# Kernel tuning notes

Hardware: AMD Instinct MI355X
Metric: run time of the kernel (lower is better)

Reference implementation:

```python
import jax, jax.numpy as jnp
import numpy as np

IN_CH = 1024
HID_CH = 1024
NUM_HEADS = 16
HEAD_DIM = HID_CH // NUM_HEADS
SCALE = (HID_CH / NUM_HEADS) ** (-0.25)


def _xavier(key, shape):
    fan_out, fan_in = shape
    limit = np.sqrt(6.0 / (fan_in + fan_out)).astype(np.float32)
    return jax.random.uniform(key, shape, jnp.float32, -limit, limit)


def setup_inputs() -> dict:
    key = jax.random.key(0)
    ks = jax.random.split(key, 5)
    B, T, L = 4, 2048, 512
    inpt = jax.random.normal(ks[0], (B, IN_CH, T), jnp.float32)
    aux = jax.random.normal(ks[1], (L, IN_CH), jnp.float32)
    q_w = _xavier(ks[2], (HID_CH, IN_CH))
    q_b = jnp.zeros((HID_CH,), jnp.float32)
    kv_w = _xavier(ks[3], (2 * HID_CH, IN_CH))
    kv_b = jnp.zeros((2 * HID_CH,), jnp.float32)
    out_w = _xavier(ks[4], (IN_CH, HID_CH))
    out_b = jnp.zeros((IN_CH,), jnp.float32)
    return {"inpt": inpt, "aux": aux, "q_w": q_w, "q_b": q_b,
            "kv_w": kv_w, "kv_b": kv_b, "out_w": out_w, "out_b": out_b}


def reference(inpt, aux, q_w, q_b, kv_w, kv_b, out_w, out_b):
    # inpt: (B, C, T), aux: (L, C)
    B, C, T = inpt.shape
    x = jnp.swapaxes(inpt, -2, -1)                     # (B, T, C)
    q = (x @ q_w.T + q_b) * SCALE                      # (B, T, H*D)
    kv = aux @ kv_w.T + kv_b                           # (L, 2*H*D)
    k, v = jnp.split(kv, 2, axis=-1)
    k = k * SCALE
    q = q.reshape(B, T, NUM_HEADS, HEAD_DIM)           # (B, T, h, d)
    L = aux.shape[0]
    k = k.reshape(L, NUM_HEADS, HEAD_DIM)              # (L, h, d)
    v = v.reshape(L, NUM_HEADS, HEAD_DIM)
    e = jnp.einsum('bihd,jhd->bijh', q, k)             # (B, T, L, h)
    attn = jax.nn.softmax(e, axis=2)                   # softmax over key axis j
    out = jnp.einsum('bijh,jhd->bihd', attn, v)        # (B, T, h, d)
    out = out.reshape(B, T, HID_CH) @ out_w.T + out_b  # (B, T, C)
    return inpt + jnp.swapaxes(out, -2, -1)            # (B, C, T)
```

## Files before the change

kernel.cpp:

```cpp
#include <hip/hip_runtime.h>
#include <cstdint>
#include <cstddef>

typedef __bf16 bf16;
typedef __bf16 bf16x4 __attribute__((ext_vector_type(4)));
typedef __bf16 bf16x8 __attribute__((ext_vector_type(8)));
typedef float f32x4 __attribute__((ext_vector_type(4)));

static constexpr float SCALE_F = 0.35355339059327373f;

#define AS1 __attribute__((address_space(1)))
#define AS3 __attribute__((address_space(3)))

__device__ __forceinline__ void load_lds16(const void* g, void* l) {
  __builtin_amdgcn_global_load_lds((AS1 void*)g, (AS3 void*)l, 16, 0, 0);
}

__global__ void prep(const float* __restrict__ q_w, bf16* __restrict__ qwb,
                     const float* __restrict__ kv_w, bf16* __restrict__ kvwb,
                     const float* __restrict__ out_w, bf16* __restrict__ owb,
                     const float* __restrict__ aux, bf16* __restrict__ auxb,
                     const float* __restrict__ inpt, bf16* __restrict__ X) {
  const int bid = blockIdx.x;
  const int tid = threadIdx.x;
  if (bid < 4608) {
    int i = bid * 256 + tid;
    const float* src;
    bf16* dst;
    int off;
    if (i < 262144) { src = q_w; dst = qwb; off = i; }
    else if (i < 786432) { src = kv_w; dst = kvwb; off = i - 262144; }
    else if (i < 1048576) { src = out_w; dst = owb; off = i - 786432; }
    else { src = aux; dst = auxb; off = i - 1048576; }
    float4 v = reinterpret_cast<const float4*>(src)[off];
    bf16x4 o;
    o[0] = (bf16)v.x; o[1] = (bf16)v.y; o[2] = (bf16)v.z; o[3] = (bf16)v.w;
    reinterpret_cast<bf16x4*>(dst)[off] = o;
  } else {
    __shared__ float tile[32][33];
    int tb = bid - 4608;
    int b = tb >> 11;
    int rem = tb & 2047;
    int c0 = (rem >> 6) * 32;
    int t0 = (rem & 63) * 32;
    int tx = tid & 31, ty = tid >> 5;
    const float* src = inpt + ((size_t)b * 1024 + c0) * 2048 + t0;
#pragma unroll
    for (int i = 0; i < 4; ++i) tile[ty + i * 8][tx] = src[(size_t)(ty + i * 8) * 2048 + tx];
    __syncthreads();
    bf16* dst = X + ((size_t)b * 2048 + t0) * 1024 + c0;
#pragma unroll
    for (int i = 0; i < 4; ++i) dst[(size_t)(ty + i * 8) * 1024 + tx] = (bf16)tile[tx][ty + i * 8];
  }
}


__global__ __launch_bounds__(256, 3) void gemm_qkv(
    const bf16* __restrict__ X, const bf16* __restrict__ qwb, const float* __restrict__ q_b,
    bf16* __restrict__ Qout, const bf16* __restrict__ auxb, const bf16* __restrict__ kvwb,
    const float* __restrict__ kv_b, bf16* __restrict__ Kout, bf16* __restrict__ Vout) {
  __shared__ __align__(16) char sA[16384];
  __shared__ __align__(16) char sB[16384];
  const int tid = threadIdx.x;
  const int lane = tid & 63;
  const int wave = tid >> 6;
  const int wm = wave >> 1, wn = wave & 1;
  const int bid = blockIdx.x;
  const bool isQ = bid < 512;
  const bf16 *A, *Bw;
  const float* bias;
  int m0, n0;
  if (isQ) {
    A = X; Bw = qwb; bias = q_b;
    m0 = (bid >> 3) * 128; n0 = (bid & 7) * 128;
  } else {
    int b2 = bid - 512;
    A = auxb; Bw = kvwb; bias = kv_b;
    m0 = (b2 & 3) * 128; n0 = (b2 >> 2) * 128;
  }
  f32x4 acc[4][4] = {};

  for (int kt = 0; kt < 1024; kt += 64) {
#pragma unroll
    for (int j = 0; j < 4; ++j) {
      int i = tid + j * 256;
      int r = i >> 3, q = i & 7;
      int so = (q ^ (r & 7)) << 4;
      load_lds16((const char*)(A + (size_t)(m0 + r) * 1024 + kt) + so, sA + (size_t)i * 16);
      load_lds16((const char*)(Bw + (size_t)(n0 + r) * 1024 + kt) + so, sB + (size_t)i * 16);
    }
    asm volatile("s_waitcnt vmcnt(0)" ::: "memory");
    __syncthreads();
    bf16x8 af[4][2], bfr[4][2];
#pragma unroll
    for (int mi = 0; mi < 4; ++mi)
#pragma unroll
      for (int kk = 0; kk < 2; ++kk) {
        int rr = wm * 64 + mi * 16 + (lane & 15);
        int w = kk * 64 + ((lane >> 4) << 4);
        af[mi][kk] = *(const bf16x8*)(sA + (size_t)rr * 128 + (w ^ ((rr & 7) << 4)));
        int r2 = wn * 64 + mi * 16 + (lane & 15);
        bfr[mi][kk] = *(const bf16x8*)(sB + (size_t)r2 * 128 + (w ^ ((r2 & 7) << 4)));
      }
#pragma unroll
    for (int kk = 0; kk < 2; ++kk)
#pragma unroll
      for (int mi = 0; mi < 4; ++mi)
#pragma unroll
        for (int ni = 0; ni < 4; ++ni)
          acc[mi][ni] =
              __builtin_amdgcn_mfma_f32_16x16x32_bf16(af[mi][kk], bfr[ni][kk], acc[mi][ni], 0, 0, 0);
    __syncthreads();
  }

  float bs[4];
#pragma unroll
  for (int ni = 0; ni < 4; ++ni) bs[ni] = bias[n0 + wn * 64 + ni * 16 + (lane & 15)];

#pragma unroll
  for (int mi = 0; mi < 4; ++mi)
#pragma unroll
    for (int ni = 0; ni < 4; ++ni)
#pragma unroll
      for (int j = 0; j < 4; ++j) {
        int row = wm * 64 + mi * 16 + ((lane >> 4) << 2) + j;
        int col = wn * 64 + ni * 16 + (lane & 15);
        int m = m0 + row, n = n0 + col;
        float val = acc[mi][ni][j] + bs[ni];
        if (isQ) {
          val *= SCALE_F;
          int bb = m >> 11, t = m & 2047, hh = n >> 6, d = n & 63;
          Qout[(((size_t)(bb * 16 + hh) * 2048 + t) << 6) + d] = (bf16)val;
        } else {
          if (n < 1024) {
            int hh = n >> 6, d = n & 63;
            Kout[(((size_t)hh * 512 + m) << 6) + d] = (bf16)(val * SCALE_F);
          } else {
            int n2 = n - 1024;
            int hh = n2 >> 6, d = n2 & 63;
            int sl = (m & 0x1E0) | (((m >> 2) & 3) << 3) | (((m >> 4) & 1) << 2) | (m & 3);
            Vout[(((size_t)hh * 64 + d) << 9) + sl] = (bf16)val;
          }
        }
      }
}

__global__ __launch_bounds__(256, 2) void gemm_outres(const bf16* __restrict__ A,
                                                      const bf16* __restrict__ Bw,
                                                      const float* __restrict__ bias,
                                                      const float* __restrict__ inpt,
                                                      float* __restrict__ out) {
  __shared__ __align__(16) char smem[65536];
  char* sA = smem;
  char* sB = smem + 16384;
  const int tid = threadIdx.x;
  const int lane = tid & 63;
  const int wave = tid >> 6;
  const int wm = wave >> 1, wn = wave & 1;
  const int g = lane >> 4, lr = lane & 15;
  const int m0 = blockIdx.x * 128, n0 = blockIdx.y * 128;
  f32x4 acc[4][4] = {};

  for (int kt = 0; kt < 1024; kt += 64) {
#pragma unroll
    for (int j = 0; j < 4; ++j) {
      int i = tid + j * 256;
      int r = i >> 3, q = i & 7;
      int so = (q ^ (r & 7)) << 4;
      load_lds16((const char*)(A + (size_t)(m0 + r) * 1024 + kt) + so, sA + (size_t)i * 16);
      load_lds16((const char*)(Bw + (size_t)(n0 + r) * 1024 + kt) + so, sB + (size_t)i * 16);
    }
    asm volatile("s_waitcnt vmcnt(0)" ::: "memory");
    __syncthreads();
    bf16x8 af[4][2], bfr[4][2];
#pragma unroll
    for (int mi = 0; mi < 4; ++mi)
#pragma unroll
      for (int kk = 0; kk < 2; ++kk) {
        int rr = wm * 64 + mi * 16 + lr;
        int w = kk * 64 + (g << 4);
        af[mi][kk] = *(const bf16x8*)(sA + (size_t)rr * 128 + (w ^ ((rr & 7) << 4)));
        int r2 = wn * 64 + mi * 16 + lr;
        bfr[mi][kk] = *(const bf16x8*)(sB + (size_t)r2 * 128 + (w ^ ((r2 & 7) << 4)));
      }
#pragma unroll
    for (int kk = 0; kk < 2; ++kk)
#pragma unroll
      for (int mi = 0; mi < 4; ++mi)
#pragma unroll
        for (int ni = 0; ni < 4; ++ni)
          acc[mi][ni] =
              __builtin_amdgcn_mfma_f32_16x16x32_bf16(af[mi][kk], bfr[ni][kk], acc[mi][ni], 0, 0, 0);
    __syncthreads();
  }

  float bs[4];
#pragma unroll
  for (int ni = 0; ni < 4; ++ni) bs[ni] = bias[n0 + wn * 64 + ni * 16 + lr];

#pragma unroll
  for (int mi = 0; mi < 4; ++mi)
#pragma unroll
    for (int ni = 0; ni < 4; ++ni) {
      int c_l = wn * 64 + ni * 16 + lr;
      int tb = (wm * 64 + mi * 16 + g * 4) * 4;
      f32x4 v;
#pragma unroll
      for (int j = 0; j < 4; ++j) v[j] = acc[mi][ni][j] + bs[ni];
      *(f32x4*)(smem + (size_t)c_l * 512 + (tb ^ ((c_l & 31) << 4))) = v;
    }
  __syncthreads();

  const int c_r = tid >> 3;
  const int tcol = (tid & 7) * 16;
  const int b = m0 >> 11, m0t = m0 & 2047;
#pragma unroll
  for (int p = 0; p < 4; ++p) {
    int c = p * 32 + c_r;
    size_t grow = ((size_t)b * 1024 + n0 + c) * 2048 + m0t;
#pragma unroll
    for (int q = 0; q < 4; ++q) {
      int t = tcol + q * 128;
      f32x4 z = *(const f32x4*)(smem + (size_t)c * 512 + (t ^ ((c & 31) << 4)));
      f32x4 iv = *(const f32x4*)(inpt + grow + (t >> 2));
      f32x4 w;
#pragma unroll
      for (int j = 0; j < 4; ++j) w[j] = iv[j] + z[j];
      *(f32x4*)(out + grow + (t >> 2)) = w;
    }
  }
}

struct Frags {
  bf16x8 ka[2][2];
  bf16x8 va[4];
};

__device__ __forceinline__ void load_frags(Frags& f, const char* lds, int G, int lr, int g) {
  const int swz = (lr & 7) << 4;
#pragma unroll
  for (int m = 0; m < 2; ++m)
#pragma unroll
    for (int kk = 0; kk < 2; ++kk)
      f.ka[m][kk] =
          *(const bf16x8*)(lds + (size_t)(G * 32 + m * 16 + lr) * 128 + ((kk * 64 + g * 16) ^ swz));
#pragma unroll
  for (int db = 0; db < 4; ++db)
    f.va[db] = *(const bf16x8*)(lds + 65536 + (size_t)(db * 16 + lr) * 1024 +
                                ((G * 64 + g * 16) ^ swz));
}

__device__ __forceinline__ void compute_group(const Frags& f, const bf16x8 (&qf)[4][2],
                                              f32x4 (&oacc)[4][4], float (&psum)[4]) {
  f32x4 sa[4][2] = {};
#pragma unroll
  for (int s = 0; s < 4; ++s)
#pragma unroll
    for (int m = 0; m < 2; ++m) {
      sa[s][m] = __builtin_amdgcn_mfma_f32_16x16x32_bf16(f.ka[m][0], qf[s][0], sa[s][m], 0, 0, 0);
      sa[s][m] = __builtin_amdgcn_mfma_f32_16x16x32_bf16(f.ka[m][1], qf[s][1], sa[s][m], 0, 0, 0);
    }
  bf16x8 pb[4];
#pragma unroll
  for (int s = 0; s < 4; ++s)
#pragma unroll
    for (int m = 0; m < 2; ++m)
#pragma unroll
      for (int j = 0; j < 4; ++j) {
        float p = __expf(sa[s][m][j] - 16.0f);
        psum[s] += p;
        pb[s][m * 4 + j] = (bf16)p;
      }
#pragma unroll
  for (int s = 0; s < 4; ++s)
#pragma unroll
    for (int db = 0; db < 4; ++db)
      oacc[s][db] = __builtin_amdgcn_mfma_f32_16x16x32_bf16(f.va[db], pb[s], oacc[s][db], 0, 0, 0);
}

__global__ __launch_bounds__(512, 2) void attn_kernel(const bf16* __restrict__ Q,
                                                      const bf16* __restrict__ Kw,
                                                      const bf16* __restrict__ Vt,
                                                      bf16* __restrict__ Y) {
  __shared__ __align__(16) char lds[131072];
  const int tid = threadIdx.x;
  const int lane = tid & 63;
  const int wv = tid >> 6;
  const int g = lane >> 4, lr = lane & 15;
  const int bix = blockIdx.x;
  const int b = bix >> 6, h = (bix >> 2) & 15, tc = bix & 3;

  const bf16* Kh = Kw + (size_t)h * 512 * 64;
  const bf16* Vh = Vt + (size_t)h * 64 * 512;
#pragma unroll
  for (int j = 0; j < 8; ++j) {
    int i = tid + j * 512;
    int r = i >> 3, c = i & 7;
    load_lds16((const char*)Kh + r * 128 + ((c * 16) ^ ((r & 7) << 4)), lds + (size_t)i * 16);
  }
#pragma unroll
  for (int j = 0; j < 8; ++j) {
    int i = tid + j * 512;
    int r = i >> 6, c = i & 63;
    load_lds16((const char*)Vh + r * 1024 + ((c * 16) ^ ((r & 7) << 4)),
               lds + 65536 + (size_t)i * 16);
  }

  const int tb = tc * 512 + wv * 64;
  const bf16* Qh = Q + ((size_t)(b * 16 + h) * 2048 + tb) * 64;
  bf16x8 qf[4][2];
#pragma unroll
  for (int s = 0; s < 4; ++s)
#pragma unroll
    for (int kk = 0; kk < 2; ++kk)
      qf[s][kk] = *(const bf16x8*)((const char*)Qh + (s * 16 + lr) * 128 + kk * 64 + g * 16);

  asm volatile("s_waitcnt vmcnt(0)" ::: "memory");
  __syncthreads();

  f32x4 oacc[4][4] = {};
  float psum[4] = {};

  Frags fA, fB;
  load_frags(fA, lds, 0, lr, g);
#pragma unroll 1
  for (int G = 0; G < 16; G += 2) {
    load_frags(fB, lds, G + 1, lr, g);
    compute_group(fA, qf, oacc, psum);
    if (G + 2 < 16) load_frags(fA, lds, G + 2, lr, g);
    compute_group(fB, qf, oacc, psum);
  }

#pragma unroll
  for (int s = 0; s < 4; ++s) {
    float ssum = psum[s];
    ssum += __shfl_xor(ssum, 16);
    ssum += __shfl_xor(ssum, 32);
    float inv = 1.0f / ssum;
    int t = tb + s * 16 + lr;
    char* yrow = (char*)Y + ((size_t)(b * 2048 + t) * 1024 + h * 64) * 2;
#pragma unroll
    for (int db = 0; db < 4; ++db) {
      bf16x4 w;
#pragma unroll
      for (int j = 0; j < 4; ++j) w[j] = (bf16)(oacc[s][db][j] * inv);
      *(bf16x4*)(yrow + (db * 16 + g * 4) * 2) = w;
    }
  }
}


extern "C" void kernel_launch(void* const* d_in, const int* in_sizes, int n_in, void* d_out,
                              int out_size, void* d_ws, size_t ws_size, hipStream_t stream) {
  const float* inpt = (const float*)d_in[0];
  const float* aux = (const float*)d_in[1];
  const float* q_w = (const float*)d_in[2];
  const float* q_b = (const float*)d_in[3];
  const float* kv_w = (const float*)d_in[4];
  const float* kv_b = (const float*)d_in[5];
  const float* out_w = (const float*)d_in[6];
  const float* out_b = (const float*)d_in[7];
  float* out = (float*)d_out;
  char* ws = (char*)d_ws;
  bf16* X = (bf16*)(ws + 0);
  bf16* QZ = (bf16*)(ws + (16u << 20));
  bf16* qwb = (bf16*)(ws + (32u << 20));
  bf16* kvwb = (bf16*)(ws + (34u << 20));
  bf16* owb = (bf16*)(ws + (38u << 20));
  bf16* auxb = (bf16*)(ws + (40u << 20));
  bf16* Kws = (bf16*)(ws + (41u << 20));
  bf16* Vtw = (bf16*)(ws + (42u << 20));

  prep<<<12800, 256, 0, stream>>>(q_w, qwb, kv_w, kvwb, out_w, owb, aux, auxb, inpt, X);
  gemm_qkv<<<576, 256, 0, stream>>>(X, qwb, q_b, QZ, auxb, kvwb, kv_b, Kws, Vtw);
  attn_kernel<<<256, 512, 0, stream>>>(QZ, Kws, Vtw, X );
  gemm_outres<<<dim3(64, 8), 256, 0, stream>>>(X, owb, out_b, inpt, out);
}
```

Baseline: 194.1 us.

## Fuse all stages into one cooperative persistent kernel with grid syncs

Replaces the four separate launches (prep, QKV GEMM, attention, output GEMM) with a single cooperative kernel of 256 blocks that uses grid.sync between phases. The KV projection converts fp32 aux and kv_w to bf16 on the fly while other blocks do the weight casts and the input transpose. The Q and output GEMMs use 256x128 tiles with double-buffered LDS staging. The aim is to remove launch gaps and intermediate round trips. The cost is fewer blocks per GEMM phase, grid-wide barrier overhead, and an unbalanced first phase.

Result: slower. 493.7 us (+154.3%).

```diff
diff --git a/kernel.cpp b/kernel.cpp
--- a/kernel.cpp
+++ b/kernel.cpp
@@ -1,6 +1,9 @@
 #include <hip/hip_runtime.h>
+#include <hip/hip_cooperative_groups.h>
 #include <cstdint>
 #include <cstddef>
+
+namespace cg = cooperative_groups;
 
 typedef __bf16 bf16;
 typedef __bf16 bf16x4 __attribute__((ext_vector_type(4)));
@@ -16,169 +19,40 @@
   __builtin_amdgcn_global_load_lds((AS1 void*)g, (AS3 void*)l, 16, 0, 0);
 }
 
-__global__ void prep(const float* __restrict__ q_w, bf16* __restrict__ qwb,
-                     const float* __restrict__ kv_w, bf16* __restrict__ kvwb,
-                     const float* __restrict__ out_w, bf16* __restrict__ owb,
-                     const float* __restrict__ aux, bf16* __restrict__ auxb,
-                     const float* __restrict__ inpt, bf16* __restrict__ X) {
-  const int bid = blockIdx.x;
-  const int tid = threadIdx.x;
-  if (bid < 4608) {
-    int i = bid * 256 + tid;
-    const float* src;
-    bf16* dst;
-    int off;
-    if (i < 262144) { src = q_w; dst = qwb; off = i; }
-    else if (i < 786432) { src = kv_w; dst = kvwb; off = i - 262144; }
-    else if (i < 1048576) { src = out_w; dst = owb; off = i - 786432; }
-    else { src = aux; dst = auxb; off = i - 1048576; }
-    float4 v = reinterpret_cast<const float4*>(src)[off];
-    bf16x4 o;
-    o[0] = (bf16)v.x; o[1] = (bf16)v.y; o[2] = (bf16)v.z; o[3] = (bf16)v.w;
-    reinterpret_cast<bf16x4*>(dst)[off] = o;
-  } else {
-    __shared__ float tile[32][33];
-    int tb = bid - 4608;
-    int b = tb >> 11;
-    int rem = tb & 2047;
-    int c0 = (rem >> 6) * 32;
-    int t0 = (rem & 63) * 32;
-    int tx = tid & 31, ty = tid >> 5;
-    const float* src = inpt + ((size_t)b * 1024 + c0) * 2048 + t0;
-#pragma unroll
-    for (int i = 0; i < 4; ++i) tile[ty + i * 8][tx] = src[(size_t)(ty + i * 8) * 2048 + tx];
-    __syncthreads();
-    bf16* dst = X + ((size_t)b * 2048 + t0) * 1024 + c0;
-#pragma unroll
-    for (int i = 0; i < 4; ++i) dst[(size_t)(ty + i * 8) * 1024 + tx] = (bf16)tile[tx][ty + i * 8];
-  }
-}
-
-
-__global__ __launch_bounds__(256, 3) void gemm_qkv(
-    const bf16* __restrict__ X, const bf16* __restrict__ qwb, const float* __restrict__ q_b,
-    bf16* __restrict__ Qout, const bf16* __restrict__ auxb, const bf16* __restrict__ kvwb,
-    const float* __restrict__ kv_b, bf16* __restrict__ Kout, bf16* __restrict__ Vout) {
-  __shared__ __align__(16) char sA[16384];
-  __shared__ __align__(16) char sB[16384];
-  const int tid = threadIdx.x;
-  const int lane = tid & 63;
-  const int wave = tid >> 6;
-  const int wm = wave >> 1, wn = wave & 1;
-  const int bid = blockIdx.x;
-  const bool isQ = bid < 512;
-  const bf16 *A, *Bw;
-  const float* bias;
-  int m0, n0;
-  if (isQ) {
-    A = X; Bw = qwb; bias = q_b;
-    m0 = (bid >> 3) * 128; n0 = (bid & 7) * 128;
-  } else {
-    int b2 = bid - 512;
-    A = auxb; Bw = kvwb; bias = kv_b;
-    m0 = (b2 & 3) * 128; n0 = (b2 >> 2) * 128;
-  }
-  f32x4 acc[4][4] = {};
-
-  for (int kt = 0; kt < 1024; kt += 64) {
+__device__ __forceinline__ void gemm_loop(char* lds, const bf16* __restrict__ A,
+                                          const bf16* __restrict__ Bw, int m0, int n0, int tid,
+                                          int lane, int wv, f32x4 (&acc)[4][4]) {
+  const int g = lane >> 4, lr = lane & 15;
+  const int wm = wv >> 1, wn = wv & 1;
+
+  auto stage = [&](int buf, int kt) {
+    char* sA = lds + buf * 49152;
+    char* sB = sA + 32768;
 #pragma unroll
     for (int j = 0; j < 4; ++j) {
-      int i = tid + j * 256;
-      int r = i >> 3, q = i & 7;
-      int so = (q ^ (r & 7)) << 4;
-      load_lds16((const char*)(A + (size_t)(m0 + r) * 1024 + kt) + so, sA + (size_t)i * 16);
-      load_lds16((const char*)(Bw + (size_t)(n0 + r) * 1024 + kt) + so, sB + (size_t)i * 16);
-    }
-    asm volatile("s_waitcnt vmcnt(0)" ::: "memory");
-    __syncthreads();
-    bf16x8 af[4][2], bfr[4][2];
-#pragma unroll
-    for (int mi = 0; mi < 4; ++mi)
-#pragma unroll
-      for (int kk = 0; kk < 2; ++kk) {
-        int rr = wm * 64 + mi * 16 + (lane & 15);
-        int w = kk * 64 + ((lane >> 4) << 4);
-        af[mi][kk] = *(const bf16x8*)(sA + (size_t)rr * 128 + (w ^ ((rr & 7) << 4)));
-        int r2 = wn * 64 + mi * 16 + (lane & 15);
-        bfr[mi][kk] = *(const bf16x8*)(sB + (size_t)r2 * 128 + (w ^ ((r2 & 7) << 4)));
-      }
-#pragma unroll
-    for (int kk = 0; kk < 2; ++kk)
-#pragma unroll
-      for (int mi = 0; mi < 4; ++mi)
-#pragma unroll
-        for (int ni = 0; ni < 4; ++ni)
-          acc[mi][ni] =
-              __builtin_amdgcn_mfma_f32_16x16x32_bf16(af[mi][kk], bfr[ni][kk], acc[mi][ni], 0, 0, 0);
-    __syncthreads();
-  }
-
-  float bs[4];
-#pragma unroll
-  for (int ni = 0; ni < 4; ++ni) bs[ni] = bias[n0 + wn * 64 + ni * 16 + (lane & 15)];
-
-#pragma unroll
-  for (int mi = 0; mi < 4; ++mi)
-#pragma unroll
-    for (int ni = 0; ni < 4; ++ni)
-#pragma unroll
-      for (int j = 0; j < 4; ++j) {
-        int row = wm * 64 + mi * 16 + ((lane >> 4) << 2) + j;
-        int col = wn * 64 + ni * 16 + (lane & 15);
-        int m = m0 + row, n = n0 + col;
-        float val = acc[mi][ni][j] + bs[ni];
-        if (isQ) {
-          val *= SCALE_F;
-          int bb = m >> 11, t = m & 2047, hh = n >> 6, d = n & 63;
-          Qout[(((size_t)(bb * 16 + hh) * 2048 + t) << 6) + d] = (bf16)val;
-        } else {
-          if (n < 1024) {
-            int hh = n >> 6, d = n & 63;
-            Kout[(((size_t)hh * 512 + m) << 6) + d] = (bf16)(val * SCALE_F);
-          } else {
-            int n2 = n - 1024;
-            int hh = n2 >> 6, d = n2 & 63;
-            int sl = (m & 0x1E0) | (((m >> 2) & 3) << 3) | (((m >> 4) & 1) << 2) | (m & 3);
-            Vout[(((size_t)hh * 64 + d) << 9) + sl] = (bf16)val;
-          }
-        }
-      }
-}
-
-__global__ __launch_bounds__(256, 2) void gemm_outres(const bf16* __restrict__ A,
-                                                      const bf16* __restrict__ Bw,
-                                                      const float* __restrict__ bias,
-                                                      const float* __restrict__ inpt,
-                                                      float* __restrict__ out) {
-  __shared__ __align__(16) char smem[65536];
-  char* sA = smem;
-  char* sB = smem + 16384;
-  const int tid = threadIdx.x;
-  const int lane = tid & 63;
-  const int wave = tid >> 6;
-  const int wm = wave >> 1, wn = wave & 1;
-  const int g = lane >> 4, lr = lane & 15;
-  const int m0 = blockIdx.x * 128, n0 = blockIdx.y * 128;
-  f32x4 acc[4][4] = {};
-
-  for (int kt = 0; kt < 1024; kt += 64) {
-#pragma unroll
-    for (int j = 0; j < 4; ++j) {
-      int i = tid + j * 256;
-      int r = i >> 3, q = i & 7;
-      int so = (q ^ (r & 7)) << 4;
-      load_lds16((const char*)(A + (size_t)(m0 + r) * 1024 + kt) + so, sA + (size_t)i * 16);
-      load_lds16((const char*)(Bw + (size_t)(n0 + r) * 1024 + kt) + so, sB + (size_t)i * 16);
-    }
-    asm volatile("s_waitcnt vmcnt(0)" ::: "memory");
-    __syncthreads();
+      int i = tid + j * 512;
+      int r = i >> 3, c = i & 7;
+      load_lds16((const char*)(A + (size_t)(m0 + r) * 1024 + kt) + ((c * 16) ^ ((r & 7) << 4)),
+                 sA + (size_t)i * 16);
+    }
+#pragma unroll
+    for (int j = 0; j < 2; ++j) {
+      int i = tid + j * 512;
+      int r = i >> 3, c = i & 7;
+      load_lds16((const char*)(Bw + (size_t)(n0 + r) * 1024 + kt) + ((c * 16) ^ ((r & 7) << 4)),
+                 sB + (size_t)i * 16);
+    }
+  };
+  auto compute = [&](int buf) {
+    char* sA = lds + buf * 49152;
+    char* sB = sA + 32768;
     bf16x8 af[4][2], bfr[4][2];
 #pragma unroll
     for (int mi = 0; mi < 4; ++mi)
 #pragma unroll
       for (int kk = 0; kk < 2; ++kk) {
         int rr = wm * 64 + mi * 16 + lr;
-        int w = kk * 64 + (g << 4);
+        int w = kk * 64 + g * 16;
         af[mi][kk] = *(const bf16x8*)(sA + (size_t)rr * 128 + (w ^ ((rr & 7) << 4)));
         int r2 = wn * 64 + mi * 16 + lr;
         bfr[mi][kk] = *(const bf16x8*)(sB + (size_t)r2 * 128 + (w ^ ((r2 & 7) << 4)));
@@ -189,46 +63,23 @@
       for (int mi = 0; mi < 4; ++mi)
 #pragma unroll
         for (int ni = 0; ni < 4; ++ni)
-          acc[mi][ni] =
-              __builtin_amdgcn_mfma_f32_16x16x32_bf16(af[mi][kk], bfr[ni][kk], acc[mi][ni], 0, 0, 0);
+          acc[mi][ni] = __builtin_amdgcn_mfma_f32_16x16x32_bf16(af[mi][kk], bfr[ni][kk],
+                                                                acc[mi][ni], 0, 0, 0);
+  };
+
+  stage(0, 0);
+  asm volatile("s_waitcnt vmcnt(0)" ::: "memory");
+  __syncthreads();
+  int cur = 0;
+#pragma unroll 1
+  for (int kt = 64; kt < 1024; kt += 64) {
+    stage(cur ^ 1, kt);
+    compute(cur);
+    asm volatile("s_waitcnt vmcnt(0)" ::: "memory");
     __syncthreads();
-  }
-
-  float bs[4];
-#pragma unroll
-  for (int ni = 0; ni < 4; ++ni) bs[ni] = bias[n0 + wn * 64 + ni * 16 + lr];
-
-#pragma unroll
-  for (int mi = 0; mi < 4; ++mi)
-#pragma unroll
-    for (int ni = 0; ni < 4; ++ni) {
-      int c_l = wn * 64 + ni * 16 + lr;
-      int tb = (wm * 64 + mi * 16 + g * 4) * 4;
-      f32x4 v;
-#pragma unroll
-      for (int j = 0; j < 4; ++j) v[j] = acc[mi][ni][j] + bs[ni];
-      *(f32x4*)(smem + (size_t)c_l * 512 + (tb ^ ((c_l & 31) << 4))) = v;
-    }
-  __syncthreads();
-
-  const int c_r = tid >> 3;
-  const int tcol = (tid & 7) * 16;
-  const int b = m0 >> 11, m0t = m0 & 2047;
-#pragma unroll
-  for (int p = 0; p < 4; ++p) {
-    int c = p * 32 + c_r;
-    size_t grow = ((size_t)b * 1024 + n0 + c) * 2048 + m0t;
-#pragma unroll
-    for (int q = 0; q < 4; ++q) {
-      int t = tcol + q * 128;
-      f32x4 z = *(const f32x4*)(smem + (size_t)c * 512 + (t ^ ((c & 31) << 4)));
-      f32x4 iv = *(const f32x4*)(inpt + grow + (t >> 2));
-      f32x4 w;
-#pragma unroll
-      for (int j = 0; j < 4; ++j) w[j] = iv[j] + z[j];
-      *(f32x4*)(out + grow + (t >> 2)) = w;
-    }
-  }
+    cur ^= 1;
+  }
+  compute(cur);
 }
 
 struct Frags {
@@ -278,16 +129,13 @@
       oacc[s][db] = __builtin_amdgcn_mfma_f32_16x16x32_bf16(f.va[db], pb[s], oacc[s][db], 0, 0, 0);
 }
 
-__global__ __launch_bounds__(512, 2) void attn_kernel(const bf16* __restrict__ Q,
-                                                      const bf16* __restrict__ Kw,
-                                                      const bf16* __restrict__ Vt,
-                                                      bf16* __restrict__ Y) {
-  __shared__ __align__(16) char lds[131072];
-  const int tid = threadIdx.x;
+__device__ __forceinline__ void attn_stage(char* lds, int bix, int tid,
+                                           const bf16* __restrict__ Q,
+                                           const bf16* __restrict__ Kw,
+                                           const bf16* __restrict__ Vt, bf16* __restrict__ Y) {
   const int lane = tid & 63;
   const int wv = tid >> 6;
   const int g = lane >> 4, lr = lane & 15;
-  const int bix = blockIdx.x;
   const int b = bix >> 6, h = (bix >> 2) & 15, tc = bix & 3;
 
   const bf16* Kh = Kw + (size_t)h * 512 * 64;
@@ -345,6 +193,202 @@
 #pragma unroll
       for (int j = 0; j < 4; ++j) w[j] = (bf16)(oacc[s][db][j] * inv);
       *(bf16x4*)(yrow + (db * 16 + g * 4) * 2) = w;
+    }
+  }
+}
+
+__global__ __launch_bounds__(512, 2) void mega(
+    const float* __restrict__ inpt, const float* __restrict__ aux, const float* __restrict__ q_w,
+    const float* __restrict__ q_b, const float* __restrict__ kv_w, const float* __restrict__ kv_b,
+    const float* __restrict__ out_w, const float* __restrict__ out_b, float* __restrict__ out,
+    bf16* __restrict__ X, bf16* __restrict__ Qb, bf16* __restrict__ qwb, bf16* __restrict__ owb,
+    bf16* __restrict__ Kws, bf16* __restrict__ Vtw) {
+  __shared__ __align__(16) char lds[131072];
+  const int tid = threadIdx.x;
+  const int bix = blockIdx.x;
+  const int lane = tid & 63, wv = tid >> 6;
+  const int g = lane >> 4, lr = lane & 15;
+  const int wm = wv >> 1, wn = wv & 1;
+  cg::grid_group grid = cg::this_grid();
+
+  if (bix >= 224) {
+    const int kb = bix - 224;
+    const int m0 = (kb & 1) * 256, n0 = (kb >> 1) * 128;
+    char* sA = lds;
+    char* sB = lds + 32768;
+    f32x4 acc[4][4] = {};
+#pragma unroll 1
+    for (int kt = 0; kt < 1024; kt += 64) {
+#pragma unroll
+      for (int j = 0; j < 8; ++j) {
+        int i = tid + j * 512;
+        int r = i >> 4, c4 = i & 15;
+        f32x4 v = *(const f32x4*)(aux + (size_t)(m0 + r) * 1024 + kt + c4 * 4);
+        bf16x4 o;
+#pragma unroll
+        for (int e = 0; e < 4; ++e) o[e] = (bf16)v[e];
+        *(bf16x4*)(sA + (size_t)r * 128 + ((c4 * 8) ^ ((r & 7) << 4))) = o;
+      }
+#pragma unroll
+      for (int j = 0; j < 4; ++j) {
+        int i = tid + j * 512;
+        int r = i >> 4, c4 = i & 15;
+        f32x4 v = *(const f32x4*)(kv_w + (size_t)(n0 + r) * 1024 + kt + c4 * 4);
+        bf16x4 o;
+#pragma unroll
+        for (int e = 0; e < 4; ++e) o[e] = (bf16)v[e];
+        *(bf16x4*)(sB + (size_t)r * 128 + ((c4 * 8) ^ ((r & 7) << 4))) = o;
+      }
+      __syncthreads();
+      bf16x8 af[4][2], bfr[4][2];
+#pragma unroll
+      for (int mi = 0; mi < 4; ++mi)
+#pragma unroll
+        for (int kk = 0; kk < 2; ++kk) {
+          int rr = wm * 64 + mi * 16 + lr;
+          int w = kk * 64 + g * 16;
+          af[mi][kk] = *(const bf16x8*)(sA + (size_t)rr * 128 + (w ^ ((rr & 7) << 4)));
+          int r2 = wn * 64 + mi * 16 + lr;
+          bfr[mi][kk] = *(const bf16x8*)(sB + (size_t)r2 * 128 + (w ^ ((r2 & 7) << 4)));
+        }
+#pragma unroll
+      for (int kk = 0; kk < 2; ++kk)
+#pragma unroll
+        for (int mi = 0; mi < 4; ++mi)
+#pragma unroll
+          for (int ni = 0; ni < 4; ++ni)
+            acc[mi][ni] = __builtin_amdgcn_mfma_f32_16x16x32_bf16(af[mi][kk], bfr[ni][kk],
+                                                                  acc[mi][ni], 0, 0, 0);
+      __syncthreads();
+    }
+    float bs[4];
+#pragma unroll
+    for (int ni = 0; ni < 4; ++ni) bs[ni] = kv_b[n0 + wn * 64 + ni * 16 + lr];
+#pragma unroll
+    for (int mi = 0; mi < 4; ++mi)
+#pragma unroll
+      for (int ni = 0; ni < 4; ++ni)
+#pragma unroll
+        for (int j = 0; j < 4; ++j) {
+          int row = wm * 64 + mi * 16 + g * 4 + j;
+          int col = wn * 64 + ni * 16 + lr;
+          int m = m0 + row, n = n0 + col;
+          float val = acc[mi][ni][j] + bs[ni];
+          if (n < 1024) {
+            int hh = n >> 6, d = n & 63;
+            Kws[(((size_t)hh * 512 + m) << 6) + d] = (bf16)(val * SCALE_F);
+          } else {
+            int n2 = n - 1024;
+            int hh = n2 >> 6, d = n2 & 63;
+            int sl = (m & 0x1E0) | (((m >> 2) & 3) << 3) | (((m >> 4) & 1) << 2) | (m & 3);
+            Vtw[(((size_t)hh * 64 + d) << 9) + sl] = (bf16)val;
+          }
+        }
+  } else {
+#pragma unroll 1
+    for (int it = 0; it < 5; ++it) {
+      int u = bix * 512 + tid + it * 114688;
+      if (u < 524288) {
+        const float* s = u < 262144 ? q_w : out_w;
+        bf16* d = u < 262144 ? qwb : owb;
+        int off = u < 262144 ? u : u - 262144;
+        float4 v = reinterpret_cast<const float4*>(s)[off];
+        bf16x4 o;
+        o[0] = (bf16)v.x; o[1] = (bf16)v.y; o[2] = (bf16)v.z; o[3] = (bf16)v.w;
+        reinterpret_cast<bf16x4*>(d)[off] = o;
+      }
+    }
+    const int team = tid >> 8, ttid = tid & 255;
+    const int tx = ttid & 31, ty = ttid >> 5;
+    float* tile = (float*)(lds + team * 4352);
+#pragma unroll 1
+    for (int it = 0; it < 19; ++it) {
+      int tix = bix * 2 + team + it * 448;
+      bool act = tix < 8192;
+      int b = tix >> 11, rem = tix & 2047;
+      int c0 = (rem >> 6) * 32, t0 = (rem & 63) * 32;
+      if (act) {
+        const float* src = inpt + ((size_t)b * 1024 + c0) * 2048 + t0;
+#pragma unroll
+        for (int i = 0; i < 4; ++i)
+          tile[(ty + i * 8) * 33 + tx] = src[(size_t)(ty + i * 8) * 2048 + tx];
+      }
+      __syncthreads();
+      if (act) {
+        bf16* dst = X + ((size_t)b * 2048 + t0) * 1024 + c0;
+#pragma unroll
+        for (int i = 0; i < 4; ++i)
+          dst[(size_t)(ty + i * 8) * 1024 + tx] = (bf16)tile[tx * 33 + ty + i * 8];
+      }
+      __syncthreads();
+    }
+  }
+  __threadfence();
+  grid.sync();
+
+  {
+    const int m0 = (bix & 31) * 256, n0 = (bix >> 5) * 128;
+    f32x4 acc[4][4] = {};
+    gemm_loop(lds, X, qwb, m0, n0, tid, lane, wv, acc);
+    float bs[4];
+#pragma unroll
+    for (int ni = 0; ni < 4; ++ni) bs[ni] = q_b[n0 + wn * 64 + ni * 16 + lr];
+#pragma unroll
+    for (int mi = 0; mi < 4; ++mi)
+#pragma unroll
+      for (int ni = 0; ni < 4; ++ni)
+#pragma unroll
+        for (int j = 0; j < 4; ++j) {
+          int row = wm * 64 + mi * 16 + g * 4 + j;
+          int col = wn * 64 + ni * 16 + lr;
+          int m = m0 + row, n = n0 + col;
+          float val = (acc[mi][ni][j] + bs[ni]) * SCALE_F;
+          int bb = m >> 11, t = m & 2047, hh = n >> 6, d = n & 63;
+          Qb[(((size_t)(bb * 16 + hh) * 2048 + t) << 6) + d] = (bf16)val;
+        }
+  }
+  __threadfence();
+  grid.sync();
+
+  attn_stage(lds, bix, tid, Qb, Kws, Vtw, X);
+  __threadfence();
+  grid.sync();
+
+  {
+    const int m0 = (bix & 31) * 256, n0 = (bix >> 5) * 128;
+    f32x4 acc[4][4] = {};
+    gemm_loop(lds, X, owb, m0, n0, tid, lane, wv, acc);
+    __syncthreads();
+
+    float bs[4];
+#pragma unroll
+    for (int ni = 0; ni < 4; ++ni) bs[ni] = out_b[n0 + wn * 64 + ni * 16 + lr];
+
+#pragma unroll
+    for (int mi = 0; mi < 4; ++mi)
+#pragma unroll
+      for (int ni = 0; ni < 4; ++ni) {
+        int c_l = wn * 64 + ni * 16 + lr;
+        int tbyt = (wm * 64 + mi * 16 + g * 4) * 4;
+        f32x4 v;
+#pragma unroll
+        for (int j = 0; j < 4; ++j) v[j] = acc[mi][ni][j] + bs[ni];
+        *(f32x4*)(lds + (size_t)c_l * 1024 + (tbyt ^ ((c_l & 15) << 4))) = v;
+      }
+    __syncthreads();
+
+    const int b = m0 >> 11, m0t = m0 & 2047;
+#pragma unroll
+    for (int q = 0; q < 16; ++q) {
+      int idx = tid + q * 512;
+      int c = idx >> 6, ch = idx & 63;
+      f32x4 z = *(const f32x4*)(lds + (size_t)c * 1024 + ((ch * 16) ^ ((c & 15) << 4)));
+      size_t fi = ((size_t)b * 1024 + n0 + c) * 2048 + m0t + ch * 4;
+      f32x4 iv = *(const f32x4*)(inpt + fi);
+      f32x4 w;
+#pragma unroll
+      for (int j = 0; j < 4; ++j) w[j] = iv[j] + z[j];
+      *(f32x4*)(out + fi) = w;
     }
   }
 }
@@ -363,16 +407,14 @@
   float* out = (float*)d_out;
   char* ws = (char*)d_ws;
   bf16* X = (bf16*)(ws + 0);
-  bf16* QZ = (bf16*)(ws + (16u << 20));
+  bf16* Qb = (bf16*)(ws + (16u << 20));
   bf16* qwb = (bf16*)(ws + (32u << 20));
-  bf16* kvwb = (bf16*)(ws + (34u << 20));
-  bf16* owb = (bf16*)(ws + (38u << 20));
-  bf16* auxb = (bf16*)(ws + (40u << 20));
-  bf16* Kws = (bf16*)(ws + (41u << 20));
-  bf16* Vtw = (bf16*)(ws + (42u << 20));
-
-  prep<<<12800, 256, 0, stream>>>(q_w, qwb, kv_w, kvwb, out_w, owb, aux, auxb, inpt, X);
-  gemm_qkv<<<576, 256, 0, stream>>>(X, qwb, q_b, QZ, auxb, kvwb, kv_b, Kws, Vtw);
-  attn_kernel<<<256, 512, 0, stream>>>(QZ, Kws, Vtw, X );
-  gemm_outres<<<dim3(64, 8), 256, 0, stream>>>(X, owb, out_b, inpt, out);
-}
+  bf16* owb = (bf16*)(ws + (34u << 20));
+  bf16* Kws = (bf16*)(ws + (36u << 20));
+  bf16* Vtw = (bf16*)(ws + (37u << 20));
+
+  void* args[] = {(void*)&inpt, (void*)&aux,  (void*)&q_w, (void*)&q_b, (void*)&kv_w,
+                  (void*)&kv_b, (void*)&out_w, (void*)&out_b, (void*)&out, (void*)&X,
+                  (void*)&Qb,   (void*)&qwb,  (void*)&owb, (void*)&Kws, (void*)&Vtw};
+  hipLaunchCooperativeKernel((void*)mega, dim3(256), dim3(512), args, 0, stream);
+}
```
